# Optimization experiments

Hardware: AMD Instinct MI355X
Metric: run time of the kernel (lower is better)

The kernel has to match this reference:

```python
import jax, jax.numpy as jnp
import numpy as np
from math import factorial

# --- constants matching init_kwargs ---
F_MM = 25.0
F_NUMBER = 2.0
PIXEL_SIZE = 3.45e-6  # meters
FOV = 32
N_ZERNIKE = 15
GRID = 256
F_M = F_MM * 1e-3
PUPIL_DIAM = F_M / F_NUMBER
BATCH = 128


def _noll_to_nm(j):
    n = 0
    k = j - 1
    while k > n:
        n += 1
        k -= n
    m = (-1) ** j * ((n % 2) + 2 * ((k + ((n + 1) % 2)) // 2))
    return n, m


def _zernike(n, m, r, theta):
    am = abs(m)
    R = np.zeros_like(r)
    for s in range((n - am) // 2 + 1):
        c = ((-1) ** s * factorial(n - s)
             / (factorial(s) * factorial((n + am) // 2 - s) * factorial((n - am) // 2 - s)))
        R = R + c * r ** (n - 2 * s)
    norm = np.sqrt(n + 1) if m == 0 else np.sqrt(2 * (n + 1))
    ang = np.cos(am * theta) if m >= 0 else np.sin(am * theta)
    return np.where(r <= 1.0, norm * R * ang, 0.0)


def _build_basis(n_modes, gs):
    lin = np.linspace(-1.0, 1.0, gs)
    y, x = np.meshgrid(lin, lin, indexing='ij')
    r = np.sqrt(x ** 2 + y ** 2)
    theta = np.arctan2(y, x)
    basis = np.stack([_zernike(*_noll_to_nm(j), r, theta) for j in range(1, n_modes + 1)]).astype(np.float32)
    aperture = (r <= 1.0).astype(np.float32)
    return basis, aperture


def _grid_sample_bilinear(img, gx, gy):
    # img: [B, G, G]; gx, gy: [H, W] in [-1,1]; align_corners=False, zero padding
    G = img.shape[-1]
    x = ((gx + 1.0) * G - 1.0) * 0.5
    y = ((gy + 1.0) * G - 1.0) * 0.5
    x0 = jnp.floor(x)
    y0 = jnp.floor(y)
    tx = x - x0
    ty = y - y0

    def tap(xf, yf, w):
        valid = (xf >= 0) & (xf <= G - 1) & (yf >= 0) & (yf <= G - 1)
        xi = jnp.clip(xf, 0, G - 1).astype(jnp.int32)
        yi = jnp.clip(yf, 0, G - 1).astype(jnp.int32)
        return img[:, yi, xi] * jnp.where(valid, w, 0.0)[None]

    return (tap(x0, y0, (1.0 - tx) * (1.0 - ty))
            + tap(x0 + 1.0, y0, tx * (1.0 - ty))
            + tap(x0, y0 + 1.0, (1.0 - tx) * ty)
            + tap(x0 + 1.0, y0 + 1.0, tx * ty))


def _compute_psf(coeffs, basis, aperture, wavelengths):
    # coeffs: [B, N]
    opd = jnp.einsum('bn,nij->bij', coeffs, basis)                     # [B,G,G]
    phase = (2.0 * np.pi) * opd[:, None] / wavelengths[None, :, None, None]  # [B,3,G,G]
    pupil = aperture * jnp.exp(1j * phase)                             # complex64
    field = jnp.fft.fftshift(jnp.fft.fft2(jnp.fft.ifftshift(pupil, axes=(-2, -1))), axes=(-2, -1))
    psf_raw = jnp.abs(field) ** 2                                      # [B,3,G,G]
    chans = []
    for i in range(3):
        zoom = PIXEL_SIZE * FOV * PUPIL_DIAM / (wavelengths[i] * F_M * GRID)
        g1 = jnp.arange(FOV, dtype=jnp.float32) / (FOV - 1) * (2.0 * zoom) - zoom  # linspace(-s, s, FOV)
        gy, gx = jnp.meshgrid(g1, g1, indexing='ij')
        chans.append(_grid_sample_bilinear(psf_raw[:, i], gx, gy))     # [B,FOV,FOV]
    psf = jnp.stack(chans, axis=1)                                     # [B,3,FOV,FOV]
    return psf / (psf.sum(axis=(-2, -1), keepdims=True) + 1e-8)


def _defocus_wfe(d_obj, d_focus):
    return F_M ** 2 / (8.0 * F_NUMBER ** 2) * (1.0 / d_focus - 1.0 / (d_obj + 1e-8))


def setup_inputs() -> dict:
    key = jax.random.key(0)
    k1, k2, k3 = jax.random.split(key, 3)
    basis, aperture = _build_basis(N_ZERNIKE, GRID)
    return {
        'd_obj': 1.0 + 4.0 * jax.random.uniform(k1, (BATCH,), dtype=jnp.float32),  # meters in [1,5)
        'current_focus_dist_0': jnp.float32(0.5),
        'current_focus_dist_90': jnp.float32(2.0),
        'zernike_0': 1e-7 * jax.random.normal(k2, (N_ZERNIKE,), dtype=jnp.float32),
        'zernike_90': 1e-7 * jax.random.normal(k3, (N_ZERNIKE,), dtype=jnp.float32),
        'zernike_basis': jnp.asarray(basis),
        'aperture': jnp.asarray(aperture),
        'wavelengths': jnp.asarray(np.array([630e-9, 550e-9, 470e-9], dtype=np.float32)),
    }


def reference(d_obj, current_focus_dist_0, current_focus_dist_90, zernike_0, zernike_90,
              zernike_basis, aperture, wavelengths):
    B = d_obj.shape[0]
    c0 = jnp.tile(zernike_0[None], (B, 1)).at[:, 3].add(_defocus_wfe(d_obj, current_focus_dist_0))
    c90 = jnp.tile(zernike_90[None], (B, 1)).at[:, 3].add(_defocus_wfe(d_obj, current_focus_dist_90))
    psf_0 = _compute_psf(c0, zernike_basis, aperture, wavelengths)
    psf_90 = _compute_psf(c90, zernike_basis, aperture, wavelengths)
    return psf_0, psf_90
```

## Files before the change

kernel.cpp:

```cpp
#include <hip/hip_runtime.h>
#include <hip/hip_bf16.h>

typedef __attribute__((ext_vector_type(8))) short short8;
typedef __attribute__((ext_vector_type(4))) float f32x4;

__device__ __forceinline__ float ldf(const float* p, long long i) { return p[i]; }
__device__ __forceinline__ float ldf(const __hip_bfloat16* p, long long i) { return __bfloat162float(p[i]); }
__device__ __forceinline__ void stf(float* p, long long i, float v) { p[i] = v; }
__device__ __forceinline__ void stf(__hip_bfloat16* p, long long i, float v) { p[i] = __float2bfloat16(v); }

__device__ __forceinline__ unsigned packbf(float a, float b) {
    unsigned ua = __float_as_uint(a), ub = __float_as_uint(b);
    ua += 0x7FFFu + ((ua >> 16) & 1u);
    ub += 0x7FFFu + ((ub >> 16) & 1u);
    return (ua >> 16) | (ub & 0xFFFF0000u);
}
__device__ __forceinline__ unsigned short bf16r(float a) {
    unsigned ua = __float_as_uint(a);
    ua += 0x7FFFu + ((ua >> 16) & 1u);
    return (unsigned short)(ua >> 16);
}
__device__ __forceinline__ unsigned cvtpk(float a, float b) {
    unsigned r;
    asm("v_cvt_pk_bf16_f32 %0, %1, %2" : "=v"(r) : "v"(a), "v"(b));
    return r;
}

union U8 { short8 h; unsigned u[4]; };

__device__ __forceinline__ f32x4 mfma16(short8 a, short8 b, f32x4 c) {
    return __builtin_amdgcn_mfma_f32_16x16x32_bf16(a, b, c, 0, 0, 0);
}

__device__ __forceinline__ bool is_bf16(const void* apraw) {
    return ((const unsigned short*)apraw)[32896] != 0;
}

template <typename ST>
__device__ __forceinline__ void prep_basis(const ST* z0, const ST* z90, const ST* basis,
        const ST* ap, const ST* wls, unsigned* ampg, float* z4g,
        float* zs, float* invl, int n, int t)
{
    if (t < 30) zs[t] = (t < 15) ? ldf(z0, t) : ldf(z90, t - 15);
    if (t >= 32 && t < 35) invl[t - 32] = (float)(1.0 / (double)ldf(wls, t - 32));
    __syncthreads();
    const int m = t;
    const int px = n * 256 + m;
    float b0 = 0.f, b90 = 0.f, z4v = 0.f;
#pragma unroll
    for (int k = 0; k < 15; ++k) {
        float bv = ldf(basis, (long long)k * 65536 + px);
        b0  = fmaf(zs[k],      bv, b0);
        b90 = fmaf(zs[15 + k], bv, b90);
        if (k == 3) z4v = bv;
    }
    float apv = ldf(ap, px);
    const int idx = ((m >> 3) * 256 + n) * 8 + (m & 7);
    z4g[idx] = z4v;
#pragma unroll
    for (int c = 0; c < 3; ++c) {
#pragma unroll
        for (int pp = 0; pp < 2; ++pp) {
            float rev = (pp ? b90 : b0) * invl[c];
            rev -= rintf(rev);
            float sn = __builtin_amdgcn_sinf(rev);
            float cs = __builtin_amdgcn_cosf(rev);
            ampg[(c * 2 + pp) * 65536 + idx] = packbf(apv * cs, apv * sn);
        }
    }
}

template <typename ST>
__device__ __forceinline__ void prep_defl(const ST* dobj, const ST* f0s, const ST* f90s,
                                          const ST* wls, float* deflg, int t)
{
#pragma unroll
    for (int k = 0; k < 3; ++k) {
        int img = k * 256 + t;
        int c = img % 3, b = (img / 3) & 127, p = img / 384;
        double lam  = (double)ldf(wls, c);
        double dfoc = (double)ldf(p ? f90s : f0s, 0);
        double dob  = (double)ldf(dobj, b);
        double def  = (0.025 * 0.025 / 32.0) * (1.0 / dfoc - 1.0 / (dob + 1e-8));
        deflg[img] = (float)(def / lam);
    }
}

__global__ void optics_prep(const void* z0, const void* z90, const void* basis,
        const void* ap, const void* wls, const void* dobj, const void* f0s, const void* f90s,
        unsigned* ampg, float* z4g, unsigned short* w2g, float* tapsw, float* deflg)
{
    __shared__ float zs[30];
    __shared__ float invl[3];
    __shared__ int tu[64];

    const bool bf = is_bf16(ap);
    const int t = threadIdx.x;
    const int blk = blockIdx.x;

    if (blk < 256) {
        if (bf) prep_basis<__hip_bfloat16>((const __hip_bfloat16*)z0, (const __hip_bfloat16*)z90,
                    (const __hip_bfloat16*)basis, (const __hip_bfloat16*)ap,
                    (const __hip_bfloat16*)wls, ampg, z4g, zs, invl, blk, t);
        else    prep_basis<float>((const float*)z0, (const float*)z90, (const float*)basis,
                    (const float*)ap, (const float*)wls, ampg, z4g, zs, invl, blk, t);
    } else if (blk < 259) {
        const int c = blk - 256;
        double lam = bf ? (double)__bfloat162float(((const __hip_bfloat16*)wls)[c])
                        : (double)((const float*)wls)[c];
        if (t < 64) {
            double zoom = (3.45e-6 * 32.0 * 0.0125) / (lam * 0.025 * 256.0);
            int s = t >> 1, a = t & 1;
            double g1 = (double)s / 31.0 * (2.0 * zoom) - zoom;
            double x  = ((g1 + 1.0) * 256.0 - 1.0) * 0.5;
            double x0 = floor(x);
            int xi = (int)x0 + a;
            float w = (float)(a ? (x - x0) : (1.0 - (x - x0)));
            tu[t] = xi - 128;
            tapsw[c * 64 + t] = (xi >= 0 && xi <= 255) ? w : 0.f;
        }
        __syncthreads();
        for (int e = 0; e < 128; ++e) {
            int entry = e * 256 + t;
            int s = entry & 15, tap = (entry >> 4) & 63, oct = entry >> 10;
            int m = oct * 8 + (s & 7);
            float rev = (float)(-tu[tap] * (m - 128)) * (1.0f / 256.0f);
            rev -= rintf(rev);
            float v = (s < 8) ? __builtin_amdgcn_cosf(rev) : __builtin_amdgcn_sinf(rev);
            w2g[c * 32768 + entry] = bf16r(v);
        }
    } else {
        if (bf) prep_defl<__hip_bfloat16>((const __hip_bfloat16*)dobj, (const __hip_bfloat16*)f0s,
                    (const __hip_bfloat16*)f90s, (const __hip_bfloat16*)wls, deflg, t);
        else    prep_defl<float>((const float*)dobj, (const float*)f0s,
                    (const float*)f90s, (const float*)wls, deflg, t);
    }
}

__global__ void __launch_bounds__(512, 4) optics_main(
    const unsigned* __restrict__ ampg, const float* __restrict__ z4g,
    const unsigned short* __restrict__ w2g, const float* __restrict__ tapsw,
    const float* __restrict__ deflg, const void* __restrict__ apraw, void* __restrict__ out)
{
    __shared__ unsigned short GlR[32 * 264];
    __shared__ unsigned short GlI[32 * 264];
    __shared__ float T[64][65];
    __shared__ float twl[64];
    __shared__ float wred[8];

    const bool bf = is_bf16(apraw);
    const int t = threadIdx.x;
    const int bid = blockIdx.x;
    const int c = bid % 3, b = (bid / 3) & 127, p = bid / 384;
    const int wave = t >> 6, lane = t & 63, li = lane & 15, g = lane >> 4;

    const float defl = deflg[bid];

    if (t < 64) twl[t] = tapsw[c * 64 + t];

    const unsigned* ampP = ampg + ((c * 2 + p) << 16);
    const short8* W2v = (const short8*)(w2g + c * 32768);

    f32x4 accR[2][4], accI[2][4];
#pragma unroll
    for (int rt = 0; rt < 2; ++rt)
#pragma unroll
        for (int vt = 0; vt < 4; ++vt) {
            accR[rt][vt] = (f32x4){0.f, 0.f, 0.f, 0.f};
            accI[rt][vt] = (f32x4){0.f, 0.f, 0.f, 0.f};
        }

    const int n0 = wave * 32;
    const int row0 = n0 + li, row1 = n0 + 16 + li;
#pragma unroll 2
    for (int ks = 0; ks < 8; ++ks) {
        const int mo = ks * 4 + g;
        const uint4*  a0p = (const uint4*)(ampP + (mo * 256 + row0) * 8);
        const uint4*  a1p = (const uint4*)(ampP + (mo * 256 + row1) * 8);
        const float4* z0p = (const float4*)(z4g + (mo * 256 + row0) * 8);
        const float4* z1p = (const float4*)(z4g + (mo * 256 + row1) * 8);
        uint4  av[2][2] = {{a0p[0], a0p[1]}, {a1p[0], a1p[1]}};
        float4 zv[2][2] = {{z0p[0], z0p[1]}, {z1p[0], z1p[1]}};

        U8 ar[2], ai[2];
#pragma unroll
        for (int rt = 0; rt < 2; ++rt) {
            float pr[8], pi[8];
#pragma unroll
            for (int jj = 0; jj < 2; ++jj)
#pragma unroll
                for (int e = 0; e < 4; ++e) {
                    const int j = jj * 4 + e;
                    unsigned a = ((const unsigned*)&av[rt][jj])[e];
                    float aRv = __uint_as_float(a << 16);
                    float aIv = __uint_as_float(a & 0xFFFF0000u);
                    float z   = ((const float*)&zv[rt][jj])[e];
                    float rev = defl * z;
                    float sn = __builtin_amdgcn_sinf(rev);
                    float cs = __builtin_amdgcn_cosf(rev);
                    pr[j] = fmaf(-aIv, sn, aRv * cs);
                    pi[j] = fmaf( aRv, sn, aIv * cs);
                }
#pragma unroll
            for (int q2 = 0; q2 < 4; ++q2) {
                ar[rt].u[q2] = cvtpk(pr[2 * q2], pr[2 * q2 + 1]);
                ai[rt].u[q2] = cvtpk(pi[2 * q2], pi[2 * q2 + 1]);
            }
        }
#pragma unroll
        for (int vt = 0; vt < 4; ++vt) {
            const short8* wp = W2v + ((mo * 64 + vt * 16 + li) << 1);
            U8 bR, bI, bN;
            bR.h = wp[0];
            bI.h = wp[1];
#pragma unroll
            for (int q2 = 0; q2 < 4; ++q2) bN.u[q2] = bI.u[q2] ^ 0x80008000u;
#pragma unroll
            for (int rt = 0; rt < 2; ++rt) {
                accR[rt][vt] = mfma16(ar[rt].h, bR.h, accR[rt][vt]);
                accR[rt][vt] = mfma16(ai[rt].h, bN.h, accR[rt][vt]);
                accI[rt][vt] = mfma16(ar[rt].h, bI.h, accI[rt][vt]);
                accI[rt][vt] = mfma16(ai[rt].h, bR.h, accI[rt][vt]);
            }
        }
    }

    const int ut = wave >> 1, vt2 = wave & 1;
#pragma unroll
    for (int h = 0; h < 2; ++h) {
        if (h) __syncthreads();
#pragma unroll
        for (int rt = 0; rt < 2; ++rt)
#pragma unroll
            for (int v2 = 0; v2 < 2; ++v2) {
                const f32x4 a = accR[rt][2 * h + v2];
                const f32x4 bb = accI[rt][2 * h + v2];
                const int off = (v2 * 16 + li) * 528 + (n0 + rt * 16 + g * 4) * 2;
                *(uint2*)((char*)GlR + off) = make_uint2(cvtpk(a[0], a[1]), cvtpk(a[2], a[3]));
                *(uint2*)((char*)GlI + off) = make_uint2(cvtpk(bb[0], bb[1]), cvtpk(bb[2], bb[3]));
            }
        __syncthreads();

        f32x4 fR = {0.f, 0.f, 0.f, 0.f}, fI = {0.f, 0.f, 0.f, 0.f};
        const int urow = ut * 16 + li;
        const int voff0 = (vt2 * 16 + li) * 528;
#pragma unroll 2
        for (int ksb = 0; ksb < 8; ++ksb) {
            const int no = ksb * 4 + g;
            const short8* wp = W2v + ((no * 64 + urow) << 1);
            U8 aWr, aWi, aWn;
            aWr.h = wp[0];
            aWi.h = wp[1];
#pragma unroll
            for (int q2 = 0; q2 < 4; ++q2) aWn.u[q2] = aWi.u[q2] ^ 0x80008000u;
            const int off = voff0 + no * 16;
            short8 gr = *(const short8*)((const char*)GlR + off);
            short8 gi = *(const short8*)((const char*)GlI + off);
            fR = mfma16(aWr.h, gr, fR);
            fR = mfma16(aWn.h, gi, fR);
            fI = mfma16(aWr.h, gi, fI);
            fI = mfma16(aWi.h, gr, fI);
        }
#pragma unroll
        for (int r = 0; r < 4; ++r)
            T[ut * 16 + g * 4 + r][h * 32 + vt2 * 16 + li] = fmaf(fR[r], fR[r], fI[r] * fI[r]);
    }
    __syncthreads();

    float vals[2]; float part = 0.f;
#pragma unroll
    for (int k = 0; k < 2; ++k) {
        int o = t + (k << 9);
        int oy = o >> 5, ox = o & 31;
        float wy0 = twl[2 * oy], wy1 = twl[2 * oy + 1];
        float wx0 = twl[2 * ox], wx1 = twl[2 * ox + 1];
        float acc = wy0 * (wx0 * T[2 * oy][2 * ox]     + wx1 * T[2 * oy][2 * ox + 1])
                  + wy1 * (wx0 * T[2 * oy + 1][2 * ox] + wx1 * T[2 * oy + 1][2 * ox + 1]);
        vals[k] = acc; part += acc;
    }
    for (int off = 32; off; off >>= 1) part += __shfl_down(part, off, 64);
    if (lane == 0) wred[wave] = part;
    __syncthreads();
    float S = 0.f;
#pragma unroll
    for (int wv = 0; wv < 8; ++wv) S += wred[wv];
    float inv = 1.f / (S + 1e-8f);
    long long obase = (long long)p * 393216 + (long long)b * 3072 + (long long)c * 1024;
    if (bf) {
        stf((__hip_bfloat16*)out, obase + t,       vals[0] * inv);
        stf((__hip_bfloat16*)out, obase + t + 512, vals[1] * inv);
    } else {
        stf((float*)out, obase + t,       vals[0] * inv);
        stf((float*)out, obase + t + 512, vals[1] * inv);
    }
}

extern "C" void kernel_launch(void* const* d_in, const int* in_sizes, int n_in,
                              void* d_out, int out_size, void* d_ws, size_t ws_size,
                              hipStream_t stream)
{
    unsigned* ampg = (unsigned*)d_ws;
    float* z4g = (float*)((char*)d_ws + 1572864);
    unsigned short* w2g = (unsigned short*)((char*)d_ws + 1835008);
    float* tapsw = (float*)((char*)d_ws + 2031616);
    float* deflg = (float*)((char*)d_ws + 2032640);

    optics_prep<<<260, 256, 0, stream>>>(
        d_in[3], d_in[4], d_in[5], d_in[6], d_in[7], d_in[0], d_in[1], d_in[2],
        ampg, z4g, w2g, tapsw, deflg);

    optics_main<<<768, 512, 0, stream>>>(
        ampg, z4g, w2g, tapsw, deflg, d_in[6], d_out);
}
```

Before: 56.40 us.

## Compute defocus phase analytically in-kernel and alias power tile onto shared buffer

```diff
diff --git a/kernel.cpp b/kernel.cpp
--- a/kernel.cpp
+++ b/kernel.cpp
@@ -138,13 +138,12 @@
 }
 
 __global__ void __launch_bounds__(512, 4) optics_main(
-    const unsigned* __restrict__ ampg, const float* __restrict__ z4g,
+    const unsigned* __restrict__ ampg,
     const unsigned short* __restrict__ w2g, const float* __restrict__ tapsw,
     const float* __restrict__ deflg, const void* __restrict__ apraw, void* __restrict__ out)
 {
     __shared__ unsigned short GlR[32 * 264];
     __shared__ unsigned short GlI[32 * 264];
-    __shared__ float T[64][65];
     __shared__ float twl[64];
     __shared__ float wred[8];
 
@@ -161,6 +160,18 @@
     const unsigned* ampP = ampg + ((c * 2 + p) << 16);
     const short8* W2v = (const short8*)(w2g + c * 32768);
 
+    const float s255 = 2.0f / 255.0f;
+    const float sq3  = 1.73205080756887729f;
+    const float Ach  = 2.0f * sq3 * defl;
+    const float Cc   = -sq3 * defl;
+
+    const int n0 = wave * 32;
+    const int row0 = n0 + li, row1 = n0 + 16 + li;
+    const float xr0 = fmaf((float)row0, s255, -1.0f);
+    const float xr1 = fmaf((float)row1, s255, -1.0f);
+    const float Brow[2] = { fmaf(Ach, xr0 * xr0, Cc), fmaf(Ach, xr1 * xr1, Cc) };
+    const float xg = fmaf((float)(g * 8), s255, -1.0f);
+
     f32x4 accR[2][4], accI[2][4];
 #pragma unroll
     for (int rt = 0; rt < 2; ++rt)
@@ -170,17 +181,13 @@
             accI[rt][vt] = (f32x4){0.f, 0.f, 0.f, 0.f};
         }
 
-    const int n0 = wave * 32;
-    const int row0 = n0 + li, row1 = n0 + 16 + li;
 #pragma unroll 2
     for (int ks = 0; ks < 8; ++ks) {
         const int mo = ks * 4 + g;
-        const uint4*  a0p = (const uint4*)(ampP + (mo * 256 + row0) * 8);
-        const uint4*  a1p = (const uint4*)(ampP + (mo * 256 + row1) * 8);
-        const float4* z0p = (const float4*)(z4g + (mo * 256 + row0) * 8);
-        const float4* z1p = (const float4*)(z4g + (mo * 256 + row1) * 8);
-        uint4  av[2][2] = {{a0p[0], a0p[1]}, {a1p[0], a1p[1]}};
-        float4 zv[2][2] = {{z0p[0], z0p[1]}, {z1p[0], z1p[1]}};
+        const float xks = fmaf((float)(ks * 32), s255, xg);
+        const uint4* a0p = (const uint4*)(ampP + (mo * 256 + row0) * 8);
+        const uint4* a1p = (const uint4*)(ampP + (mo * 256 + row1) * 8);
+        uint4 av[2][2] = {{a0p[0], a0p[1]}, {a1p[0], a1p[1]}};
 
         U8 ar[2], ai[2];
 #pragma unroll
@@ -194,8 +201,8 @@
                     unsigned a = ((const unsigned*)&av[rt][jj])[e];
                     float aRv = __uint_as_float(a << 16);
                     float aIv = __uint_as_float(a & 0xFFFF0000u);
-                    float z   = ((const float*)&zv[rt][jj])[e];
-                    float rev = defl * z;
+                    const float xm = xks + (float)j * s255;
+                    const float rev = fmaf(Ach, xm * xm, Brow[rt]);
                     float sn = __builtin_amdgcn_sinf(rev);
                     float cs = __builtin_amdgcn_cosf(rev);
                     pr[j] = fmaf(-aIv, sn, aRv * cs);
@@ -226,6 +233,7 @@
     }
 
     const int ut = wave >> 1, vt2 = wave & 1;
+    f32x4 p4[2];
 #pragma unroll
     for (int h = 0; h < 2; ++h) {
         if (h) __syncthreads();
@@ -261,10 +269,15 @@
             fI = mfma16(aWr.h, gi, fI);
             fI = mfma16(aWi.h, gr, fI);
         }
+        p4[h] = fR * fR + fI * fI;
+    }
+    __syncthreads();
+    float* T = (float*)GlR;
+#pragma unroll
+    for (int h = 0; h < 2; ++h)
 #pragma unroll
         for (int r = 0; r < 4; ++r)
-            T[ut * 16 + g * 4 + r][h * 32 + vt2 * 16 + li] = fmaf(fR[r], fR[r], fI[r] * fI[r]);
-    }
+            T[(ut * 16 + g * 4 + r) * 65 + h * 32 + vt2 * 16 + li] = p4[h][r];
     __syncthreads();
 
     float vals[2]; float part = 0.f;
@@ -274,8 +287,8 @@
         int oy = o >> 5, ox = o & 31;
         float wy0 = twl[2 * oy], wy1 = twl[2 * oy + 1];
         float wx0 = twl[2 * ox], wx1 = twl[2 * ox + 1];
-        float acc = wy0 * (wx0 * T[2 * oy][2 * ox]     + wx1 * T[2 * oy][2 * ox + 1])
-                  + wy1 * (wx0 * T[2 * oy + 1][2 * ox] + wx1 * T[2 * oy + 1][2 * ox + 1]);
+        float acc = wy0 * (wx0 * T[(2 * oy) * 65 + 2 * ox]     + wx1 * T[(2 * oy) * 65 + 2 * ox + 1])
+                  + wy1 * (wx0 * T[(2 * oy + 1) * 65 + 2 * ox] + wx1 * T[(2 * oy + 1) * 65 + 2 * ox + 1]);
         vals[k] = acc; part += acc;
     }
     for (int off = 32; off; off >>= 1) part += __shfl_down(part, off, 64);
@@ -310,5 +323,5 @@
         ampg, z4g, w2g, tapsw, deflg);
 
     optics_main<<<768, 512, 0, stream>>>(
-        ampg, z4g, w2g, tapsw, deflg, d_in[6], d_out);
-}
+        ampg, w2g, tapsw, deflg, d_in[6], d_out);
+}
```

After: 53.62 us (median of 2 runs). -4.9%, faster.
